# Kernel optimization log

Measured on AMD Instinct MI355X. Metric: run time of the kernel, lower is better.

Reference implementation:

```python
import jax, jax.numpy as jnp
import numpy as np

MAP_DS = 2.0
H, W = 512, 1024
MAXENT_WEIGHT = 1.0
EPS = 1e-5


def setup_inputs() -> dict:
    key = jax.random.key(0)
    k1, k2, k3 = jax.random.split(key, 3)
    B, T = 64, 256
    # Bounded random-walk trajectories in world coords (x in [0, H*ds), y in [0, W*ds))
    steps = jax.random.uniform(k1, (B, T, 2), minval=0.0, maxval=4.0)
    xy = jnp.cumsum(steps, axis=1) + 50.0
    xy = jnp.stack([jnp.clip(xy[..., 0], 0.0, H * MAP_DS - 1.0),
                    jnp.clip(xy[..., 1], 0.0, W * MAP_DS - 1.0)], axis=-1)
    # Pack into SE(2) pose matrices [B, T, 3, 3] with translation in [:2, 2]
    gt = jnp.tile(jnp.eye(3, dtype=jnp.float32), (B, T, 1, 1))
    gt = gt.at[:, :, 0, 2].set(xy[..., 0]).at[:, :, 1, 2].set(xy[..., 1])
    exp_svf = jax.random.uniform(k2, (B, H, W), dtype=jnp.float32)
    reward_preds = jax.random.normal(k3, (B, H, W), dtype=jnp.float32)
    return {"gt": gt, "exp_svf": exp_svf, "reward_preds": reward_preds}


def compute_expert_visitation(gt, max_steps):
    # gt: [B, T, 3, 3] SE(2) poses
    B = gt.shape[0]
    xy = gt[:, :, :2, 2] / MAP_DS                       # [B, T, 2] grid coords
    start = xy[:, :-1]                                  # [B, T-1, 2]
    end = xy[:, 1:]                                     # [B, T-1, 2]
    t = jnp.linspace(0.0, 1.0, max_steps, dtype=xy.dtype).reshape(1, 1, -1, 1)
    pts = start[:, :, None, :] + t * (end - start)[:, :, None, :]   # [B, T-1, S, 2]
    pts = pts.reshape(B, -1, 2)
    pts = jnp.concatenate([pts, xy[:, -1:]], axis=1)    # append last pose -> [B, N, 2]
    x = jnp.clip(pts[:, :, 0], 0, H - 1).astype(jnp.int32)
    y = jnp.clip(pts[:, :, 1], 0, W - 1).astype(jnp.int32)
    lin = x * W + y                                     # [B, N] flat indices
    flat = jnp.zeros((B, H * W), dtype=jnp.float32)
    flat = flat.at[jnp.arange(B)[:, None], lin].add(1.0)  # scatter-add histogram
    counts = jnp.minimum(flat, 1.0).reshape(B, H, W)      # binarize visitation
    return pts, counts


def reference(gt, exp_svf, reward_preds):
    # max_steps from concrete data, mirroring torch's .item() (eager, not traced)
    xy = np.asarray(gt)[:, :, :2, 2] / MAP_DS
    dist = np.linalg.norm(xy[:, 1:] - xy[:, :-1], axis=-1)
    max_steps = int(np.ceil(dist).max())
    interp_pts, svf = compute_expert_visitation(gt, max_steps)
    svf = svf / (svf.sum(axis=(1, 2), keepdims=True) + EPS)
    exp_svf = exp_svf / (exp_svf.sum(axis=(1, 2), keepdims=True) + EPS)
    svf_rewards = (svf * reward_preds).sum(axis=(1, 2))         # [B]
    exp_svf_rewards = (exp_svf * reward_preds).sum(axis=(1, 2))  # [B]
    visitation_loss = exp_svf_rewards.mean() - svf_rewards.mean()
    loss = MAXENT_WEIGHT * visitation_loss
    return loss, svf, interp_pts
```

## Files before the change

### kernel.cpp

```cpp
#include <hip/hip_runtime.h>

#define Bb 64
#define Tt 256
#define Hh 512
#define Ww 1024
#define HW (Hh * Ww)
#define EPSF 1e-5f

#define SB Bb
#define RB 2048
#define CHUNK 16384

typedef float vf4 __attribute__((ext_vector_type(4)));


__device__ __forceinline__ void comp_pt(const float* __restrict__ gt, int b,
                                        int idx, int ms, int segN,
                                        float& px, float& py) {
    if (idx < segN) {
        int seg = idx / ms;
        int k = idx - seg * ms;
        const float* g0 = gt + (size_t)(b * Tt + seg) * 9;
        float sx = g0[2] * 0.5f, sy = g0[5] * 0.5f;
        float ex = g0[11] * 0.5f, ey = g0[14] * 0.5f;
        float t = (ms > 1) ? (float)k / (float)(ms - 1) : 0.0f;
        px = __fadd_rn(sx, __fmul_rn(t, __fsub_rn(ex, sx)));
        py = __fadd_rn(sy, __fmul_rn(t, __fsub_rn(ey, sy)));
    } else {
        const float* g0 = gt + (size_t)(b * Tt + (Tt - 1)) * 9;
        px = g0[2] * 0.5f;
        py = g0[5] * 0.5f;
    }
}

__device__ __forceinline__ int pt_cell(float px, float py) {
    int xi = (int)fminf(fmaxf(px, 0.0f), (float)(Hh - 1));
    int yi = (int)fminf(fmaxf(py, 0.0f), (float)(Ww - 1));
    return xi * Ww + yi;
}

__global__ __launch_bounds__(256) void combined_kernel(
        const float* __restrict__ exps, const float* __restrict__ rew,
        const float* __restrict__ gt,
        float* __restrict__ pts, float* __restrict__ svf,
        double* __restrict__ esum_p, double* __restrict__ edot_p,
        int* __restrict__ count_out, double* __restrict__ vdot_out,
        int ms, int P) {
    int segN = (Tt - 1) * ms;

    if (blockIdx.x < SB) {
        int b = blockIdx.x;

        int myCount = 0;
        float myV = 0.0f;
        for (int idx = threadIdx.x; idx < P; idx += 256) {
            float px, py;
            comp_pt(gt, b, idx, ms, segN, px, py);
            size_t pi = ((size_t)b * P + idx) * 2;
            pts[pi]     = px;
            pts[pi + 1] = py;
            int cell = pt_cell(px, py);
            bool claim;
            if (idx == 0) {
                claim = true;
            } else {
                float qx, qy;
                comp_pt(gt, b, idx - 1, ms, segN, qx, qy);
                claim = (pt_cell(qx, qy) != cell);
            }
            if (claim) {
                myCount++;
                myV += rew[(size_t)b * HW + cell];
            }
        }

        for (int off = 32; off; off >>= 1) {
            myCount += __shfl_down(myCount, off);
            myV     += __shfl_down(myV, off);
        }
        __shared__ int   sc[4];
        __shared__ float sv[4];
        int lane = threadIdx.x & 63, wv = threadIdx.x >> 6;
        if (lane == 0) { sc[wv] = myCount; sv[wv] = myV; }
        __syncthreads();
        if (threadIdx.x == 0) {
            int tot  = (sc[0] + sc[1]) + (sc[2] + sc[3]);
            float tv = (sv[0] + sv[1]) + (sv[2] + sv[3]);
            count_out[b] = tot;
            vdot_out[b]  = (double)tv;
        }
    } else {
        int blk = blockIdx.x - SB;
        int b = blk >> 5;
        int c = blk & 31;
        size_t base = (size_t)b * HW + (size_t)c * CHUNK;

        {
            float* p = svf + base;
            int head = (int)((16 - ((uintptr_t)p & 15)) & 15) >> 2;
            int nv   = (CHUNK - head) >> 2;
            int tail = CHUNK - head - (nv << 2);
            if ((int)threadIdx.x < head) p[threadIdx.x] = 0.0f;
            if ((int)threadIdx.x < tail) p[head + (nv << 2) + threadIdx.x] = 0.0f;
            vf4* v4 = (vf4*)(p + head);
            vf4 z = {0.0f, 0.0f, 0.0f, 0.0f};
            for (int k = (int)threadIdx.x; k < nv; k += 256) v4[k] = z;
        }

        float es = 0.0f, ed = 0.0f;
        #pragma unroll
        for (int j = 0; j < 2; ++j) {
            const vf4* e4 = (const vf4*)(exps + base) + j * 2048 + threadIdx.x;
            const vf4* r4 = (const vf4*)(rew  + base) + j * 2048 + threadIdx.x;
            vf4 ev[8], rv[8];
            #pragma unroll
            for (int k = 0; k < 8; ++k) ev[k] = e4[k * 256];
            #pragma unroll
            for (int k = 0; k < 8; ++k) rv[k] = r4[k * 256];
            #pragma unroll
            for (int k = 0; k < 8; ++k) {
                vf4 e = ev[k], r = rv[k];
                es += (e.x + e.y) + (e.z + e.w);
                ed += (e.x * r.x + e.y * r.y) + (e.z * r.z + e.w * r.w);
            }
        }
        for (int off = 32; off; off >>= 1) {
            es += __shfl_down(es, off);
            ed += __shfl_down(ed, off);
        }

        int myCount = 0;
        for (int idx = threadIdx.x; idx < P; idx += 256) {
            float px, py;
            comp_pt(gt, b, idx, ms, segN, px, py);
            int cell = pt_cell(px, py);
            bool claim;
            if (idx == 0) {
                claim = true;
            } else {
                float qx, qy;
                comp_pt(gt, b, idx - 1, ms, segN, qx, qy);
                claim = (pt_cell(qx, qy) != cell);
            }
            myCount += claim ? 1 : 0;
        }
        for (int off = 32; off; off >>= 1) myCount += __shfl_down(myCount, off);

        __shared__ float s_es[4], s_ed[4];
        __shared__ int   sc2[4];
        int lane = threadIdx.x & 63, wv = threadIdx.x >> 6;
        if (lane == 0) { s_es[wv] = es; s_ed[wv] = ed; sc2[wv] = myCount; }
        __syncthreads();
        if (threadIdx.x == 0) {
            esum_p[blk] = (double)((s_es[0] + s_es[1]) + (s_es[2] + s_es[3]));
            edot_p[blk] = (double)((s_ed[0] + s_ed[1]) + (s_ed[2] + s_ed[3]));
        }
        int tot = (sc2[0] + sc2[1]) + (sc2[2] + sc2[3]);
        float recip = 1.0f / ((float)tot + EPSF);

        int lo = c * CHUNK, hi = lo + CHUNK;
        for (int idx = threadIdx.x; idx < P; idx += 256) {
            float px, py;
            comp_pt(gt, b, idx, ms, segN, px, py);
            int cell = pt_cell(px, py);
            if (cell >= lo && cell < hi)
                svf[(size_t)b * HW + cell] = recip;
        }
    }
}

__global__ void loss_kernel(const double* __restrict__ esum_p,
                            const double* __restrict__ edot_p,
                            const double* __restrict__ vdot,
                            const int* __restrict__ count,
                            float* __restrict__ loss_out) {
    int b = threadIdx.x;
    double es = 0.0, ed = 0.0;
    #pragma unroll 8
    for (int c = 0; c < 32; ++c) {
        es += esum_p[b * 32 + c];
        ed += edot_p[b * 32 + c];
    }
    double e = ed / (es + 1e-5);
    double v = vdot[b] / ((double)count[b] + 1e-5);
    double term = e - v;
    for (int off = 32; off; off >>= 1) term += __shfl_down(term, off);
    if (b == 0) loss_out[0] = (float)(term / (double)Bb);
}

extern "C" void kernel_launch(void* const* d_in, const int* in_sizes, int n_in,
                              void* d_out, int out_size, void* d_ws, size_t ws_size,
                              hipStream_t stream) {
    const float* gt   = (const float*)d_in[0];
    const float* exps = (const float*)d_in[1];
    const float* rew  = (const float*)d_in[2];
    float* out = (float*)d_out;

    float* loss_out = out;
    float* svf = out + 1;
    int P  = (out_size - 1 - Bb * HW) / (Bb * 2);
    int ms = (P - 1) / (Tt - 1);
    float* pts = out + 1 + (size_t)Bb * HW;

    int*    count  = (int*)d_ws;
    double* vdot   = (double*)((char*)d_ws + 256);
    double* esum_p = (double*)((char*)d_ws + 768);
    double* edot_p = (double*)((char*)d_ws + 17152);

    combined_kernel<<<SB + RB, 256, 0, stream>>>(exps, rew, gt, pts, svf,
                                                 esum_p, edot_p, count, vdot,
                                                 ms, P);
    loss_kernel<<<1, 64, 0, stream>>>(esum_p, edot_p, vdot, count, loss_out);
}
```

Before: 326.3 us.

## Fold per-batch scatter blocks into reduction blocks and use nontemporal stores

Removes the separate 64 per-batch blocks and assigns their work (writing interpolated points and the reward gather for claimed cells) to one reduction block per batch, chosen on a rotating chunk index. All streaming writes (svf zero fill, point output, svf scatter) switch to nontemporal stores so the large output does not pollute cache. This cuts the grid to 2048 uniform blocks and drops the tail of long-running scatter blocks. The trade-off is that one block per batch now does extra work, which may lengthen its critical path.

```diff
diff --git a/kernel.cpp b/kernel.cpp
--- a/kernel.cpp
+++ b/kernel.cpp
@@ -7,7 +7,6 @@
 #define HW (Hh * Ww)
 #define EPSF 1e-5f
 
-#define SB Bb
 #define RB 2048
 #define CHUNK 16384
 
@@ -46,126 +45,103 @@
         double* __restrict__ esum_p, double* __restrict__ edot_p,
         int* __restrict__ count_out, double* __restrict__ vdot_out,
         int ms, int P) {
+    int blk = blockIdx.x;
+    int b = blk >> 5;
+    int c = blk & 31;
+    bool isScat = (c == (b & 31));
     int segN = (Tt - 1) * ms;
+    size_t base = (size_t)b * HW + (size_t)c * CHUNK;
 
-    if (blockIdx.x < SB) {
-        int b = blockIdx.x;
+    {
+        float* p = svf + base;
+        int head = (int)((16 - ((uintptr_t)p & 15)) & 15) >> 2;
+        int nv   = (CHUNK - head) >> 2;
+        int tail = CHUNK - head - (nv << 2);
+        if ((int)threadIdx.x < head)
+            __builtin_nontemporal_store(0.0f, p + threadIdx.x);
+        if ((int)threadIdx.x < tail)
+            __builtin_nontemporal_store(0.0f, p + head + (nv << 2) + threadIdx.x);
+        vf4* v4 = (vf4*)(p + head);
+        vf4 z = {0.0f, 0.0f, 0.0f, 0.0f};
+        for (int k = (int)threadIdx.x; k < nv; k += 256)
+            __builtin_nontemporal_store(z, v4 + k);
+    }
 
-        int myCount = 0;
-        float myV = 0.0f;
-        for (int idx = threadIdx.x; idx < P; idx += 256) {
-            float px, py;
-            comp_pt(gt, b, idx, ms, segN, px, py);
+    float es = 0.0f, ed = 0.0f;
+    #pragma unroll
+    for (int j = 0; j < 2; ++j) {
+        const vf4* e4 = (const vf4*)(exps + base) + j * 2048 + threadIdx.x;
+        const vf4* r4 = (const vf4*)(rew  + base) + j * 2048 + threadIdx.x;
+        vf4 ev[8], rv[8];
+        #pragma unroll
+        for (int k = 0; k < 8; ++k) ev[k] = e4[k * 256];
+        #pragma unroll
+        for (int k = 0; k < 8; ++k) rv[k] = r4[k * 256];
+        #pragma unroll
+        for (int k = 0; k < 8; ++k) {
+            vf4 e = ev[k], r = rv[k];
+            es += (e.x + e.y) + (e.z + e.w);
+            ed += (e.x * r.x + e.y * r.y) + (e.z * r.z + e.w * r.w);
+        }
+    }
+    for (int off = 32; off; off >>= 1) {
+        es += __shfl_down(es, off);
+        ed += __shfl_down(ed, off);
+    }
+
+    int myCount = 0;
+    float myV = 0.0f;
+    for (int idx = threadIdx.x; idx < P; idx += 256) {
+        float px, py;
+        comp_pt(gt, b, idx, ms, segN, px, py);
+        int cell = pt_cell(px, py);
+        bool claim;
+        if (idx == 0) {
+            claim = true;
+        } else {
+            float qx, qy;
+            comp_pt(gt, b, idx - 1, ms, segN, qx, qy);
+            claim = (pt_cell(qx, qy) != cell);
+        }
+        myCount += claim ? 1 : 0;
+        if (isScat) {
             size_t pi = ((size_t)b * P + idx) * 2;
-            pts[pi]     = px;
-            pts[pi + 1] = py;
-            int cell = pt_cell(px, py);
-            bool claim;
-            if (idx == 0) {
-                claim = true;
-            } else {
-                float qx, qy;
-                comp_pt(gt, b, idx - 1, ms, segN, qx, qy);
-                claim = (pt_cell(qx, qy) != cell);
-            }
-            if (claim) {
-                myCount++;
-                myV += rew[(size_t)b * HW + cell];
-            }
+            __builtin_nontemporal_store(px, pts + pi);
+            __builtin_nontemporal_store(py, pts + pi + 1);
+            if (claim) myV += rew[(size_t)b * HW + cell];
         }
+    }
+    for (int off = 32; off; off >>= 1) {
+        myCount += __shfl_down(myCount, off);
+        myV     += __shfl_down(myV, off);
+    }
 
-        for (int off = 32; off; off >>= 1) {
-            myCount += __shfl_down(myCount, off);
-            myV     += __shfl_down(myV, off);
-        }
-        __shared__ int   sc[4];
-        __shared__ float sv[4];
-        int lane = threadIdx.x & 63, wv = threadIdx.x >> 6;
-        if (lane == 0) { sc[wv] = myCount; sv[wv] = myV; }
-        __syncthreads();
-        if (threadIdx.x == 0) {
-            int tot  = (sc[0] + sc[1]) + (sc[2] + sc[3]);
+    __shared__ float s_es[4], s_ed[4];
+    __shared__ float sv[4];
+    __shared__ int   sc2[4];
+    int lane = threadIdx.x & 63, wv = threadIdx.x >> 6;
+    if (lane == 0) { s_es[wv] = es; s_ed[wv] = ed; sc2[wv] = myCount; sv[wv] = myV; }
+    __syncthreads();
+    if (threadIdx.x == 0) {
+        esum_p[blk] = (double)((s_es[0] + s_es[1]) + (s_es[2] + s_es[3]));
+        edot_p[blk] = (double)((s_ed[0] + s_ed[1]) + (s_ed[2] + s_ed[3]));
+        if (isScat) {
+            int tot  = (sc2[0] + sc2[1]) + (sc2[2] + sc2[3]);
             float tv = (sv[0] + sv[1]) + (sv[2] + sv[3]);
             count_out[b] = tot;
             vdot_out[b]  = (double)tv;
         }
-    } else {
-        int blk = blockIdx.x - SB;
-        int b = blk >> 5;
-        int c = blk & 31;
-        size_t base = (size_t)b * HW + (size_t)c * CHUNK;
+    }
+    int tot = (sc2[0] + sc2[1]) + (sc2[2] + sc2[3]);
+    float recip = 1.0f / ((float)tot + EPSF);
 
-        {
-            float* p = svf + base;
-            int head = (int)((16 - ((uintptr_t)p & 15)) & 15) >> 2;
-            int nv   = (CHUNK - head) >> 2;
-            int tail = CHUNK - head - (nv << 2);
-            if ((int)threadIdx.x < head) p[threadIdx.x] = 0.0f;
-            if ((int)threadIdx.x < tail) p[head + (nv << 2) + threadIdx.x] = 0.0f;
-            vf4* v4 = (vf4*)(p + head);
-            vf4 z = {0.0f, 0.0f, 0.0f, 0.0f};
-            for (int k = (int)threadIdx.x; k < nv; k += 256) v4[k] = z;
-        }
-
-        float es = 0.0f, ed = 0.0f;
-        #pragma unroll
-        for (int j = 0; j < 2; ++j) {
-            const vf4* e4 = (const vf4*)(exps + base) + j * 2048 + threadIdx.x;
-            const vf4* r4 = (const vf4*)(rew  + base) + j * 2048 + threadIdx.x;
-            vf4 ev[8], rv[8];
-            #pragma unroll
-            for (int k = 0; k < 8; ++k) ev[k] = e4[k * 256];
-            #pragma unroll
-            for (int k = 0; k < 8; ++k) rv[k] = r4[k * 256];
-            #pragma unroll
-            for (int k = 0; k < 8; ++k) {
-                vf4 e = ev[k], r = rv[k];
-                es += (e.x + e.y) + (e.z + e.w);
-                ed += (e.x * r.x + e.y * r.y) + (e.z * r.z + e.w * r.w);
-            }
-        }
-        for (int off = 32; off; off >>= 1) {
-            es += __shfl_down(es, off);
-            ed += __shfl_down(ed, off);
-        }
-
-        int myCount = 0;
-        for (int idx = threadIdx.x; idx < P; idx += 256) {
-            float px, py;
-            comp_pt(gt, b, idx, ms, segN, px, py);
-            int cell = pt_cell(px, py);
-            bool claim;
-            if (idx == 0) {
-                claim = true;
-            } else {
-                float qx, qy;
-                comp_pt(gt, b, idx - 1, ms, segN, qx, qy);
-                claim = (pt_cell(qx, qy) != cell);
-            }
-            myCount += claim ? 1 : 0;
-        }
-        for (int off = 32; off; off >>= 1) myCount += __shfl_down(myCount, off);
-
-        __shared__ float s_es[4], s_ed[4];
-        __shared__ int   sc2[4];
-        int lane = threadIdx.x & 63, wv = threadIdx.x >> 6;
-        if (lane == 0) { s_es[wv] = es; s_ed[wv] = ed; sc2[wv] = myCount; }
-        __syncthreads();
-        if (threadIdx.x == 0) {
-            esum_p[blk] = (double)((s_es[0] + s_es[1]) + (s_es[2] + s_es[3]));
-            edot_p[blk] = (double)((s_ed[0] + s_ed[1]) + (s_ed[2] + s_ed[3]));
-        }
-        int tot = (sc2[0] + sc2[1]) + (sc2[2] + sc2[3]);
-        float recip = 1.0f / ((float)tot + EPSF);
-
-        int lo = c * CHUNK, hi = lo + CHUNK;
-        for (int idx = threadIdx.x; idx < P; idx += 256) {
-            float px, py;
-            comp_pt(gt, b, idx, ms, segN, px, py);
-            int cell = pt_cell(px, py);
-            if (cell >= lo && cell < hi)
-                svf[(size_t)b * HW + cell] = recip;
-        }
+    int lo = c * CHUNK, hi = lo + CHUNK;
+    for (int idx = threadIdx.x; idx < P; idx += 256) {
+        float px, py;
+        comp_pt(gt, b, idx, ms, segN, px, py);
+        int cell = pt_cell(px, py);
+        if (cell >= lo && cell < hi)
+            __builtin_nontemporal_store(recip, svf + (size_t)b * HW + cell);
     }
 }
 
@@ -207,8 +183,8 @@
     double* esum_p = (double*)((char*)d_ws + 768);
     double* edot_p = (double*)((char*)d_ws + 17152);
 
-    combined_kernel<<<SB + RB, 256, 0, stream>>>(exps, rew, gt, pts, svf,
-                                                 esum_p, edot_p, count, vdot,
-                                                 ms, P);
+    combined_kernel<<<RB, 256, 0, stream>>>(exps, rew, gt, pts, svf,
+                                            esum_p, edot_p, count, vdot,
+                                            ms, P);
     loss_kernel<<<1, 64, 0, stream>>>(esum_p, edot_p, vdot, count, loss_out);
 }
```

Result: slower. 340.4 us (+4.3%).
